# Kernel tuning notes

Measured on AMD Instinct MI355X. Metric: run time of the kernel, lower is better.

The kernel has to match this reference:

```python
import jax, jax.numpy as jnp
import numpy as np

N_NODES = 50000


def _gcn_layer(h_in, src, dst, norm, W, b, n_nodes):
    # PyG GCNConv: linear transform, then normalized scatter-add aggregation.
    h = h_in @ W                                   # [N, out]
    msg = h[src] * norm[:, None]                   # gather + scale, [E+N, out]
    out = jax.ops.segment_sum(msg, dst, num_segments=n_nodes)  # scatter-add
    return out + b


def _self_loop_norm(edge_index, n_nodes):
    # Add self loops, compute symmetric normalization deg^-1/2 (row) * deg^-1/2 (col).
    loop = jnp.arange(n_nodes, dtype=edge_index.dtype)
    src = jnp.concatenate([edge_index[0], loop])
    dst = jnp.concatenate([edge_index[1], loop])
    deg = jax.ops.segment_sum(jnp.ones_like(dst, dtype=jnp.float32), dst,
                              num_segments=n_nodes)
    dinv = jnp.where(deg > 0, jax.lax.rsqrt(deg), 0.0)
    norm = dinv[src] * dinv[dst]                   # [E+N]
    return src, dst, norm


def setup_inputs() -> dict:
    key = jax.random.key(0)
    ks = jax.random.split(key, 8)
    in_c, hid, out_c = 128, 64, 16
    x = jax.random.normal(ks[0], (N_NODES, in_c), dtype=jnp.float32)
    edge_index = jax.random.randint(ks[1], (2, 800000), 0, N_NODES, dtype=jnp.int64)
    def lin(k, fan_in, fan_out):
        lim = 1.0 / np.sqrt(fan_in)
        return jax.random.uniform(k, (fan_in, fan_out), jnp.float32, -lim, lim)
    return {
        "x": x,
        "edge_index": edge_index,
        "W1": lin(ks[2], in_c, hid), "b1": jnp.zeros((hid,), jnp.float32),
        "W2": lin(ks[3], hid, hid), "b2": jnp.zeros((hid,), jnp.float32),
        "Wm1": lin(ks[4], 2 * hid, hid), "bm1": jnp.zeros((hid,), jnp.float32),
        "Wm2": lin(ks[5], hid, out_c), "bm2": jnp.zeros((out_c,), jnp.float32),
    }


def reference(x, edge_index, W1, b1, W2, b2, Wm1, bm1, Wm2, bm2):
    n_nodes = x.shape[0]
    src, dst, norm = _self_loop_norm(edge_index, n_nodes)
    h = jax.nn.relu(_gcn_layer(x, src, dst, norm, W1, b1, n_nodes))
    h = jax.nn.relu(_gcn_layer(h, src, dst, norm, W2, b2, n_nodes))
    row, col = edge_index[0], edge_index[1]
    ef = jnp.concatenate([h[row], h[col]], axis=1)   # [E, 2*hid]
    z = jax.nn.relu(ef @ Wm1 + bm1)
    return z @ Wm2 + bm2
```

## Files before the change

kernel.cpp:

```cpp
#include <hip/hip_runtime.h>
#include <hip/hip_bf16.h>


#define IN_C 128
#define HID 64
#define OUT_C 16

__device__ __forceinline__ float rlanef(float v, int l) {
    return __uint_as_float(__builtin_amdgcn_readlane(__float_as_uint(v), l));
}


__global__ void k_init_cnt(int* __restrict__ cnt, int n) {
    int i = blockIdx.x * blockDim.x + threadIdx.x;
    if (i < n) cnt[i] = 0;
}

__global__ void k_count(const int* __restrict__ ei, int* __restrict__ cnt, int e) {
    int i = blockIdx.x * blockDim.x + threadIdx.x;
    if (i < e) atomicAdd(&cnt[ei[e + i]], 1);
}

__global__ __launch_bounds__(1024) void k_scan1(const int* __restrict__ cnt,
                                                int* __restrict__ tmp,
                                                int* __restrict__ bsum, int n) {
    __shared__ int s[1024];
    int i = blockIdx.x * 1024 + threadIdx.x;
    int v = (i < n) ? cnt[i] : 0;
    s[threadIdx.x] = v;
    __syncthreads();
    for (int off = 1; off < 1024; off <<= 1) {
        int add = (threadIdx.x >= off) ? s[threadIdx.x - off] : 0;
        __syncthreads();
        s[threadIdx.x] += add;
        __syncthreads();
    }
    if (i < n) tmp[i] = s[threadIdx.x];
    if (threadIdx.x == 1023) bsum[blockIdx.x] = s[1023];
}

__global__ __launch_bounds__(64) void k_scan2(int* __restrict__ bsum, int nb) {
    int lane = threadIdx.x;
    int v = (lane < nb) ? bsum[lane] : 0;
    int orig = v;
    for (int off = 1; off < 64; off <<= 1) {
        int t = __shfl_up(v, off, 64);
        if (lane >= off) v += t;
    }
    if (lane < nb) bsum[lane] = v - orig;
}

__global__ void k_scan3(const int* __restrict__ cnt, const int* __restrict__ tmp,
                        const int* __restrict__ bsum, int* __restrict__ rowptr,
                        int* __restrict__ cur, float* __restrict__ dinv, int n, int e) {
    int i = blockIdx.x * blockDim.x + threadIdx.x;
    if (i < n) {
        int excl = tmp[i] - cnt[i] + bsum[i >> 10];
        rowptr[i] = excl;
        cur[i] = excl;
        dinv[i] = 1.0f / sqrtf((float)(cnt[i] + 1));
        if (i == 0) rowptr[n] = e;
    }
}

__global__ void k_scatter(const int* __restrict__ ei, int* __restrict__ cur,
                          int* __restrict__ csrc, int2* __restrict__ cde, int e) {
    int i = blockIdx.x * blockDim.x + threadIdx.x;
    if (i < e) {
        int s = ei[i];
        int d = ei[e + i];
        int p = atomicAdd(&cur[d], 1);
        csrc[p] = s;
        cde[p] = make_int2(d, i);
    }
}


template <int K>
__global__ __launch_bounds__(256) void k_gemm_node(const float* __restrict__ A,
                                                   const float* __restrict__ W,
                                                   const float* __restrict__ dinv,
                                                   float* __restrict__ T,
                                                   int n, int npw) {
    int lane = threadIdx.x & 63;
    int w = threadIdx.x >> 6;
    float wr[K];
#pragma unroll
    for (int k = 0; k < K; ++k) wr[k] = W[k * 64 + lane];
    int gw = blockIdx.x * 4 + w;
    int n0 = gw * npw;
    int n1 = n0 + npw; if (n1 > n) n1 = n;
#pragma unroll 1
    for (int i = n0; i < n1; ++i) {
        float a0 = A[(size_t)i * K + lane];
        float a1 = 0.f;
        if (K == 128) a1 = A[(size_t)i * K + 64 + lane];
        float acc = 0.f;
#pragma unroll
        for (int k = 0; k < 64; ++k) acc = fmaf(rlanef(a0, k), wr[k], acc);
        if (K == 128) {
#pragma unroll
            for (int k = 0; k < 64; ++k) acc = fmaf(rlanef(a1, k), wr[64 + k], acc);
        }
        T[(size_t)i * 64 + lane] = acc * dinv[i];
    }
}

__global__ __launch_bounds__(256) void k_gemm_uv(const float* __restrict__ Hm,
                                                 const float* __restrict__ Wm1,
                                                 const float* __restrict__ bm1,
                                                 float* __restrict__ ut,
                                                 float* __restrict__ vt,
                                                 int n, int npw) {
    int lane = threadIdx.x & 63;
    int w = threadIdx.x >> 6;
    float wu[64], wv[64];
#pragma unroll
    for (int k = 0; k < 64; ++k) wu[k] = Wm1[k * 64 + lane];
#pragma unroll
    for (int k = 0; k < 64; ++k) wv[k] = Wm1[(64 + k) * 64 + lane];
    float bv = bm1[lane];
    int gw = blockIdx.x * 4 + w;
    int n0 = gw * npw;
    int n1 = n0 + npw; if (n1 > n) n1 = n;
#pragma unroll 1
    for (int i = n0; i < n1; ++i) {
        float a0 = Hm[(size_t)i * 64 + lane];
        float au = 0.f, av = 0.f;
#pragma unroll
        for (int k = 0; k < 64; ++k) {
            float hb = rlanef(a0, k);
            au = fmaf(hb, wu[k], au);
            av = fmaf(hb, wv[k], av);
        }
        ut[(size_t)i * 64 + lane] = au;
        vt[(size_t)i * 64 + lane] = av + bv;
    }
}


__device__ __forceinline__ float4 agg_gather(const float* __restrict__ T,
                                             const int* __restrict__ rowptr,
                                             const int* __restrict__ csrc,
                                             float dn, float4 b4,
                                             int nid, int g, int c4) {
    float4 acc = make_float4(0.f, 0.f, 0.f, 0.f);
    if (g == 0) {
        acc = *(const float4*)(T + (size_t)nid * 64 + 4 * c4);
    }
    int r0 = rowptr[nid], r1 = rowptr[nid + 1];
#pragma unroll 1
    for (int p = r0 + g; p < r1; p += 4) {
        int s = csrc[p];
        float4 t = *(const float4*)(T + (size_t)s * 64 + 4 * c4);
        acc.x += t.x; acc.y += t.y; acc.z += t.z; acc.w += t.w;
    }
    acc.x += __shfl_xor(acc.x, 16, 64); acc.y += __shfl_xor(acc.y, 16, 64);
    acc.z += __shfl_xor(acc.z, 16, 64); acc.w += __shfl_xor(acc.w, 16, 64);
    acc.x += __shfl_xor(acc.x, 32, 64); acc.y += __shfl_xor(acc.y, 32, 64);
    acc.z += __shfl_xor(acc.z, 32, 64); acc.w += __shfl_xor(acc.w, 32, 64);
    float4 h;
    h.x = fmaxf(fmaf(dn, acc.x, b4.x), 0.f);
    h.y = fmaxf(fmaf(dn, acc.y, b4.y), 0.f);
    h.z = fmaxf(fmaf(dn, acc.z, b4.z), 0.f);
    h.w = fmaxf(fmaf(dn, acc.w, b4.w), 0.f);
    return h;
}

__global__ __launch_bounds__(256) void k_agg_l1(const float* __restrict__ T,
                                                const int* __restrict__ rowptr,
                                                const int* __restrict__ csrc,
                                                const float* __restrict__ dinv,
                                                const float* __restrict__ bias,
                                                const float* __restrict__ W2,
                                                float* __restrict__ T2,
                                                int n, int npw) {
    int lane = threadIdx.x & 63;
    int w = threadIdx.x >> 6;
    int g = lane >> 4, c4 = lane & 15;
    float wr[64];
#pragma unroll
    for (int k = 0; k < 64; ++k) wr[k] = W2[k * 64 + lane];
    float4 b4 = ((const float4*)bias)[c4];
    int gw = blockIdx.x * 4 + w;
    int n0 = gw * npw;
    int n1 = n0 + npw; if (n1 > n) n1 = n;
#pragma unroll 1
    for (int nid = n0; nid < n1; ++nid) {
        float dn = dinv[nid];
        float4 h = agg_gather(T, rowptr, csrc, dn, b4, nid, g, c4);
        float acc2 = 0.f;
#pragma unroll
        for (int q = 0; q < 16; ++q) {
            acc2 = fmaf(rlanef(h.x, q), wr[4 * q + 0], acc2);
            acc2 = fmaf(rlanef(h.y, q), wr[4 * q + 1], acc2);
            acc2 = fmaf(rlanef(h.z, q), wr[4 * q + 2], acc2);
            acc2 = fmaf(rlanef(h.w, q), wr[4 * q + 3], acc2);
        }
        T2[(size_t)nid * 64 + lane] = acc2 * dn;
    }
}

__global__ __launch_bounds__(256) void k_agg_l2(const float* __restrict__ T,
                                                const int* __restrict__ rowptr,
                                                const int* __restrict__ csrc,
                                                const float* __restrict__ dinv,
                                                const float* __restrict__ bias,
                                                float* __restrict__ H,
                                                int n, int npw) {
    int lane = threadIdx.x & 63;
    int w = threadIdx.x >> 6;
    int g = lane >> 4, c4 = lane & 15;
    float4 b4 = ((const float4*)bias)[c4];
    int gw = blockIdx.x * 4 + w;
    int n0 = gw * npw;
    int n1 = n0 + npw; if (n1 > n) n1 = n;
#pragma unroll 1
    for (int nid = n0; nid < n1; ++nid) {
        float dn = dinv[nid];
        float4 h = agg_gather(T, rowptr, csrc, dn, b4, nid, g, c4);
        if (g == 0) *(float4*)(H + (size_t)nid * 64 + 4 * c4) = h;
    }
}


#define RELUADD4(zq, uq, vq) \
    zq.x = fmaxf(uq.x + vq.x, 0.f); zq.y = fmaxf(uq.y + vq.y, 0.f); \
    zq.z = fmaxf(uq.z + vq.z, 0.f); zq.w = fmaxf(uq.w + vq.w, 0.f);

#define S2Q(zs, j) { \
    const float* w2 = Wm2 + (size_t)(j) * 16; \
    o0.x = fmaf(zs, w2[0],  o0.x);  o0.y = fmaf(zs, w2[1],  o0.y); \
    o0.z = fmaf(zs, w2[2],  o0.z);  o0.w = fmaf(zs, w2[3],  o0.w); \
    o1.x = fmaf(zs, w2[4],  o1.x);  o1.y = fmaf(zs, w2[5],  o1.y); \
    o1.z = fmaf(zs, w2[6],  o1.z);  o1.w = fmaf(zs, w2[7],  o1.w); \
    o2.x = fmaf(zs, w2[8],  o2.x);  o2.y = fmaf(zs, w2[9],  o2.y); \
    o2.z = fmaf(zs, w2[10], o2.z);  o2.w = fmaf(zs, w2[11], o2.w); \
    o3.x = fmaf(zs, w2[12], o3.x);  o3.y = fmaf(zs, w2[13], o3.y); \
    o3.z = fmaf(zs, w2[14], o3.z);  o3.w = fmaf(zs, w2[15], o3.w); }

__global__ __launch_bounds__(256, 4) void k_mlp(const float* __restrict__ ut,
                                                const float* __restrict__ vt,
                                                const int* __restrict__ csrc,
                                                const int2* __restrict__ cde,
                                                const float* __restrict__ Wm2,
                                                const float* __restrict__ bm2,
                                                float* __restrict__ out,
                                                int e) {
    int p = blockIdx.x * 256 + threadIdx.x;
    bool ok = p < e;
    int idx = ok ? p : 0;
    int r = csrc[idx];
    int2 cv = cde[idx];
    int c  = cv.x;
    int eo = cv.y;

    const float4* uq = (const float4*)(ut + (size_t)r * 64);
    const float4* vq = (const float4*)(vt + (size_t)c * 64);

    float4 u0 = uq[0],  u1 = uq[1],  u2 = uq[2],  u3 = uq[3];
    float4 u4 = uq[4],  u5 = uq[5],  u6 = uq[6],  u7 = uq[7];
    float4 u8 = uq[8],  u9 = uq[9],  u10 = uq[10], u11 = uq[11];
    float4 u12 = uq[12], u13 = uq[13], u14 = uq[14], u15 = uq[15];
    float4 v0 = vq[0],  v1 = vq[1],  v2 = vq[2],  v3 = vq[3];
    float4 v4 = vq[4],  v5 = vq[5],  v6 = vq[6],  v7 = vq[7];
    float4 v8 = vq[8],  v9 = vq[9],  v10 = vq[10], v11 = vq[11];
    float4 v12 = vq[12], v13 = vq[13], v14 = vq[14], v15 = vq[15];

    float4 z0, z1, z2, z3, z4, z5, z6, z7, z8, z9, z10, z11, z12, z13, z14, z15;
    RELUADD4(z0, u0, v0)    RELUADD4(z1, u1, v1)    RELUADD4(z2, u2, v2)    RELUADD4(z3, u3, v3)
    RELUADD4(z4, u4, v4)    RELUADD4(z5, u5, v5)    RELUADD4(z6, u6, v6)    RELUADD4(z7, u7, v7)
    RELUADD4(z8, u8, v8)    RELUADD4(z9, u9, v9)    RELUADD4(z10, u10, v10) RELUADD4(z11, u11, v11)
    RELUADD4(z12, u12, v12) RELUADD4(z13, u13, v13) RELUADD4(z14, u14, v14) RELUADD4(z15, u15, v15)

    const float4* b2q = (const float4*)bm2;
    float4 o0 = b2q[0], o1 = b2q[1], o2 = b2q[2], o3 = b2q[3];

    S2Q(z0.x, 0)   S2Q(z0.y, 1)   S2Q(z0.z, 2)   S2Q(z0.w, 3)
    S2Q(z1.x, 4)   S2Q(z1.y, 5)   S2Q(z1.z, 6)   S2Q(z1.w, 7)
    S2Q(z2.x, 8)   S2Q(z2.y, 9)   S2Q(z2.z, 10)  S2Q(z2.w, 11)
    S2Q(z3.x, 12)  S2Q(z3.y, 13)  S2Q(z3.z, 14)  S2Q(z3.w, 15)
    S2Q(z4.x, 16)  S2Q(z4.y, 17)  S2Q(z4.z, 18)  S2Q(z4.w, 19)
    S2Q(z5.x, 20)  S2Q(z5.y, 21)  S2Q(z5.z, 22)  S2Q(z5.w, 23)
    S2Q(z6.x, 24)  S2Q(z6.y, 25)  S2Q(z6.z, 26)  S2Q(z6.w, 27)
    S2Q(z7.x, 28)  S2Q(z7.y, 29)  S2Q(z7.z, 30)  S2Q(z7.w, 31)
    S2Q(z8.x, 32)  S2Q(z8.y, 33)  S2Q(z8.z, 34)  S2Q(z8.w, 35)
    S2Q(z9.x, 36)  S2Q(z9.y, 37)  S2Q(z9.z, 38)  S2Q(z9.w, 39)
    S2Q(z10.x, 40) S2Q(z10.y, 41) S2Q(z10.z, 42) S2Q(z10.w, 43)
    S2Q(z11.x, 44) S2Q(z11.y, 45) S2Q(z11.z, 46) S2Q(z11.w, 47)
    S2Q(z12.x, 48) S2Q(z12.y, 49) S2Q(z12.z, 50) S2Q(z12.w, 51)
    S2Q(z13.x, 52) S2Q(z13.y, 53) S2Q(z13.z, 54) S2Q(z13.w, 55)
    S2Q(z14.x, 56) S2Q(z14.y, 57) S2Q(z14.z, 58) S2Q(z14.w, 59)
    S2Q(z15.x, 60) S2Q(z15.y, 61) S2Q(z15.z, 62) S2Q(z15.w, 63)

    if (ok) {
        float4* op = (float4*)(out + (size_t)eo * 16);
        op[0] = o0; op[1] = o1; op[2] = o2; op[3] = o3;
    }
}


extern "C" void kernel_launch(void* const* d_in, const int* in_sizes, int n_in,
                              void* d_out, int out_size, void* d_ws, size_t ws_size,
                              hipStream_t stream) {
    const float* x   = (const float*)d_in[0];
    const int*   ei  = (const int*)d_in[1];
    const float* W1  = (const float*)d_in[2];
    const float* b1  = (const float*)d_in[3];
    const float* W2  = (const float*)d_in[4];
    const float* b2  = (const float*)d_in[5];
    const float* Wm1 = (const float*)d_in[6];
    const float* bm1 = (const float*)d_in[7];
    const float* Wm2 = (const float*)d_in[8];
    const float* bm2 = (const float*)d_in[9];
    float* out = (float*)d_out;

    int n = in_sizes[0] / IN_C;
    int e = in_sizes[1] / 2;

    char* w = (char*)d_ws;
    int* cnt    = (int*)w;                 w += (size_t)n * 4;
    int* tmp    = (int*)w;                 w += (size_t)n * 4;
    int* bsum   = (int*)w;                 w += 256 * 4;
    int* rowptr = (int*)w;                 w += (size_t)(n + 4) * 4;
    int* cur    = (int*)w;                 w += (size_t)n * 4;
    float* dinv = (float*)w;               w += (size_t)n * 4;
    int* csrc   = (int*)w;                 w += (size_t)e * 4;
    int2* cde   = (int2*)w;                w += (size_t)e * 8;
    float* t1   = (float*)w;               w += (size_t)n * HID * 4;
    float* t2   = (float*)w;               w += (size_t)n * HID * 4;
    float* h2   = (float*)w;               w += (size_t)n * HID * 4;
    float* ut   = t1;
    float* vt   = t2;

    int nb_n256 = (n + 255) / 256;
    int nb_e256 = (e + 255) / 256;
    int nb_scan = (n + 1023) / 1024;

    k_init_cnt<<<nb_n256, 256, 0, stream>>>(cnt, n);
    k_count<<<nb_e256, 256, 0, stream>>>(ei, cnt, e);
    k_scan1<<<nb_scan, 1024, 0, stream>>>(cnt, tmp, bsum, n);
    k_scan2<<<1, 64, 0, stream>>>(bsum, nb_scan);
    k_scan3<<<nb_n256, 256, 0, stream>>>(cnt, tmp, bsum, rowptr, cur, dinv, n, e);
    k_scatter<<<nb_e256, 256, 0, stream>>>(ei, cur, csrc, cde, e);

    const int NPW = 8;
    int nwaves = (n + NPW - 1) / NPW;
    int nb_gemm = (nwaves + 3) / 4;
    const int NPB = 8;
    int nb_agg = (n + 4 * NPB - 1) / (4 * NPB);

    k_gemm_node<IN_C><<<nb_gemm, 256, 0, stream>>>(x, W1, dinv, t1, n, NPW);
    k_agg_l1<<<nb_agg, 256, 0, stream>>>(t1, rowptr, csrc, dinv, b1, W2, t2, n, NPB);
    k_agg_l2<<<nb_agg, 256, 0, stream>>>(t2, rowptr, csrc, dinv, b2, h2, n, NPB);
    k_gemm_uv<<<nb_gemm, 256, 0, stream>>>(h2, Wm1, bm1, ut, vt, n, NPW);
    int nb_mlp = (e + 255) / 256;
    k_mlp<<<nb_mlp, 256, 0, stream>>>(ut, vt, csrc, cde, Wm2, bm2, out, e);
}
```

Measured before the change: 327.7 us.

## Fuse layer-2 aggregation with Wm1 projection, unroll gather, retune occupancy

Merges the second GCN aggregation with the per-node u/v projection through Wm1, so the separate k_gemm_uv launch and the h2 round trip through global memory go away. The neighbour gather loop is unrolled by four to keep more loads in flight. In the layer-1 and fused kernels, weights are now read from memory inside the loop instead of being held in 64 registers per lane, trading register pressure for repeated (cached) loads. Nodes per wave drop from 8 to 4 and the MLP kernel's launch bounds rise to 8 blocks, both aimed at higher occupancy at the risk of register spills.

```diff
diff --git a/kernel.cpp b/kernel.cpp
--- a/kernel.cpp
+++ b/kernel.cpp
@@ -106,38 +106,6 @@
     }
 }
 
-__global__ __launch_bounds__(256) void k_gemm_uv(const float* __restrict__ Hm,
-                                                 const float* __restrict__ Wm1,
-                                                 const float* __restrict__ bm1,
-                                                 float* __restrict__ ut,
-                                                 float* __restrict__ vt,
-                                                 int n, int npw) {
-    int lane = threadIdx.x & 63;
-    int w = threadIdx.x >> 6;
-    float wu[64], wv[64];
-#pragma unroll
-    for (int k = 0; k < 64; ++k) wu[k] = Wm1[k * 64 + lane];
-#pragma unroll
-    for (int k = 0; k < 64; ++k) wv[k] = Wm1[(64 + k) * 64 + lane];
-    float bv = bm1[lane];
-    int gw = blockIdx.x * 4 + w;
-    int n0 = gw * npw;
-    int n1 = n0 + npw; if (n1 > n) n1 = n;
-#pragma unroll 1
-    for (int i = n0; i < n1; ++i) {
-        float a0 = Hm[(size_t)i * 64 + lane];
-        float au = 0.f, av = 0.f;
-#pragma unroll
-        for (int k = 0; k < 64; ++k) {
-            float hb = rlanef(a0, k);
-            au = fmaf(hb, wu[k], au);
-            av = fmaf(hb, wv[k], av);
-        }
-        ut[(size_t)i * 64 + lane] = au;
-        vt[(size_t)i * 64 + lane] = av + bv;
-    }
-}
-
 
 __device__ __forceinline__ float4 agg_gather(const float* __restrict__ T,
                                              const int* __restrict__ rowptr,
@@ -149,8 +117,24 @@
         acc = *(const float4*)(T + (size_t)nid * 64 + 4 * c4);
     }
     int r0 = rowptr[nid], r1 = rowptr[nid + 1];
-#pragma unroll 1
-    for (int p = r0 + g; p < r1; p += 4) {
+    int p = r0 + g;
+#pragma unroll 1
+    for (; p + 12 < r1; p += 16) {
+        int s0 = csrc[p];
+        int s1 = csrc[p + 4];
+        int s2 = csrc[p + 8];
+        int s3 = csrc[p + 12];
+        float4 t0 = *(const float4*)(T + (size_t)s0 * 64 + 4 * c4);
+        float4 t1 = *(const float4*)(T + (size_t)s1 * 64 + 4 * c4);
+        float4 t2 = *(const float4*)(T + (size_t)s2 * 64 + 4 * c4);
+        float4 t3 = *(const float4*)(T + (size_t)s3 * 64 + 4 * c4);
+        acc.x += (t0.x + t1.x) + (t2.x + t3.x);
+        acc.y += (t0.y + t1.y) + (t2.y + t3.y);
+        acc.z += (t0.z + t1.z) + (t2.z + t3.z);
+        acc.w += (t0.w + t1.w) + (t2.w + t3.w);
+    }
+#pragma unroll 1
+    for (; p < r1; p += 4) {
         int s = csrc[p];
         float4 t = *(const float4*)(T + (size_t)s * 64 + 4 * c4);
         acc.x += t.x; acc.y += t.y; acc.z += t.z; acc.w += t.w;
@@ -178,9 +162,6 @@
     int lane = threadIdx.x & 63;
     int w = threadIdx.x >> 6;
     int g = lane >> 4, c4 = lane & 15;
-    float wr[64];
-#pragma unroll
-    for (int k = 0; k < 64; ++k) wr[k] = W2[k * 64 + lane];
     float4 b4 = ((const float4*)bias)[c4];
     int gw = blockIdx.x * 4 + w;
     int n0 = gw * npw;
@@ -190,28 +171,32 @@
         float dn = dinv[nid];
         float4 h = agg_gather(T, rowptr, csrc, dn, b4, nid, g, c4);
         float acc2 = 0.f;
-#pragma unroll
+#pragma unroll 4
         for (int q = 0; q < 16; ++q) {
-            acc2 = fmaf(rlanef(h.x, q), wr[4 * q + 0], acc2);
-            acc2 = fmaf(rlanef(h.y, q), wr[4 * q + 1], acc2);
-            acc2 = fmaf(rlanef(h.z, q), wr[4 * q + 2], acc2);
-            acc2 = fmaf(rlanef(h.w, q), wr[4 * q + 3], acc2);
+            acc2 = fmaf(rlanef(h.x, q), W2[(4 * q + 0) * 64 + lane], acc2);
+            acc2 = fmaf(rlanef(h.y, q), W2[(4 * q + 1) * 64 + lane], acc2);
+            acc2 = fmaf(rlanef(h.z, q), W2[(4 * q + 2) * 64 + lane], acc2);
+            acc2 = fmaf(rlanef(h.w, q), W2[(4 * q + 3) * 64 + lane], acc2);
         }
         T2[(size_t)nid * 64 + lane] = acc2 * dn;
     }
 }
 
-__global__ __launch_bounds__(256) void k_agg_l2(const float* __restrict__ T,
-                                                const int* __restrict__ rowptr,
-                                                const int* __restrict__ csrc,
-                                                const float* __restrict__ dinv,
-                                                const float* __restrict__ bias,
-                                                float* __restrict__ H,
-                                                int n, int npw) {
+__global__ __launch_bounds__(256) void k_agg_l2uv(const float* __restrict__ T,
+                                                  const int* __restrict__ rowptr,
+                                                  const int* __restrict__ csrc,
+                                                  const float* __restrict__ dinv,
+                                                  const float* __restrict__ bias,
+                                                  const float* __restrict__ Wm1,
+                                                  const float* __restrict__ bm1,
+                                                  float* __restrict__ ut,
+                                                  float* __restrict__ vt,
+                                                  int n, int npw) {
     int lane = threadIdx.x & 63;
     int w = threadIdx.x >> 6;
     int g = lane >> 4, c4 = lane & 15;
     float4 b4 = ((const float4*)bias)[c4];
+    float bv = bm1[lane];
     int gw = blockIdx.x * 4 + w;
     int n0 = gw * npw;
     int n1 = n0 + npw; if (n1 > n) n1 = n;
@@ -219,7 +204,24 @@
     for (int nid = n0; nid < n1; ++nid) {
         float dn = dinv[nid];
         float4 h = agg_gather(T, rowptr, csrc, dn, b4, nid, g, c4);
-        if (g == 0) *(float4*)(H + (size_t)nid * 64 + 4 * c4) = h;
+        float au = 0.f, av = 0.f;
+#pragma unroll 4
+        for (int q = 0; q < 16; ++q) {
+            float h0 = rlanef(h.x, q);
+            float h1 = rlanef(h.y, q);
+            float h2 = rlanef(h.z, q);
+            float h3 = rlanef(h.w, q);
+            au = fmaf(h0, Wm1[(4 * q + 0) * 64 + lane], au);
+            au = fmaf(h1, Wm1[(4 * q + 1) * 64 + lane], au);
+            au = fmaf(h2, Wm1[(4 * q + 2) * 64 + lane], au);
+            au = fmaf(h3, Wm1[(4 * q + 3) * 64 + lane], au);
+            av = fmaf(h0, Wm1[(64 + 4 * q + 0) * 64 + lane], av);
+            av = fmaf(h1, Wm1[(64 + 4 * q + 1) * 64 + lane], av);
+            av = fmaf(h2, Wm1[(64 + 4 * q + 2) * 64 + lane], av);
+            av = fmaf(h3, Wm1[(64 + 4 * q + 3) * 64 + lane], av);
+        }
+        ut[(size_t)nid * 64 + lane] = au;
+        vt[(size_t)nid * 64 + lane] = av + bv;
     }
 }
 
@@ -239,7 +241,7 @@
     o3.x = fmaf(zs, w2[12], o3.x);  o3.y = fmaf(zs, w2[13], o3.y); \
     o3.z = fmaf(zs, w2[14], o3.z);  o3.w = fmaf(zs, w2[15], o3.w); }
 
-__global__ __launch_bounds__(256, 4) void k_mlp(const float* __restrict__ ut,
+__global__ __launch_bounds__(256, 8) void k_mlp(const float* __restrict__ ut,
                                                 const float* __restrict__ vt,
                                                 const int* __restrict__ csrc,
                                                 const int2* __restrict__ cde,
@@ -329,9 +331,8 @@
     int2* cde   = (int2*)w;                w += (size_t)e * 8;
     float* t1   = (float*)w;               w += (size_t)n * HID * 4;
     float* t2   = (float*)w;               w += (size_t)n * HID * 4;
-    float* h2   = (float*)w;               w += (size_t)n * HID * 4;
+    float* vt   = (float*)w;               w += (size_t)n * HID * 4;
     float* ut   = t1;
-    float* vt   = t2;
 
     int nb_n256 = (n + 255) / 256;
     int nb_e256 = (e + 255) / 256;
@@ -347,13 +348,13 @@
     const int NPW = 8;
     int nwaves = (n + NPW - 1) / NPW;
     int nb_gemm = (nwaves + 3) / 4;
-    const int NPB = 8;
+    const int NPB = 4;
     int nb_agg = (n + 4 * NPB - 1) / (4 * NPB);
 
     k_gemm_node<IN_C><<<nb_gemm, 256, 0, stream>>>(x, W1, dinv, t1, n, NPW);
     k_agg_l1<<<nb_agg, 256, 0, stream>>>(t1, rowptr, csrc, dinv, b1, W2, t2, n, NPB);
-    k_agg_l2<<<nb_agg, 256, 0, stream>>>(t2, rowptr, csrc, dinv, b2, h2, n, NPB);
-    k_gemm_uv<<<nb_gemm, 256, 0, stream>>>(h2, Wm1, bm1, ut, vt, n, NPW);
+    k_agg_l2uv<<<nb_agg, 256, 0, stream>>>(t2, rowptr, csrc, dinv, b2, Wm1, bm1,
+                                           ut, vt, n, NPB);
     int nb_mlp = (e + 255) / 256;
     k_mlp<<<nb_mlp, 256, 0, stream>>>(ut, vt, csrc, cde, Wm2, bm2, out, e);
 }
```

Result: slower. 357.3 us (+9.0%).
